# Kernel tuning notes

Measured on AMD Instinct MI355X. Metric: run time of the kernel, lower is better.

Reference implementation:

```python
import jax, jax.numpy as jnp
import numpy as np
from jax import lax

B, T, I, H = 64, 512, 512, 1024


def setup_inputs() -> dict:
    key = jax.random.key(0)
    k1, k2, k3, k4 = jax.random.split(key, 4)
    # Gates stacked in order: resetgate, updategate, hidden_update (matches forward()).
    inp = jax.random.normal(k1, (B, T, I), dtype=jnp.float32)
    W_in_stacked = jax.random.normal(k2, (I, 3 * H), dtype=jnp.float32) * 0.1
    W_hid_stacked = jax.random.normal(k3, (H, 3 * H), dtype=jnp.float32) * 0.1
    b_stacked = jax.random.normal(k4, (3 * H,), dtype=jnp.float32) * 0.1
    hid_init = jnp.zeros((1, H), dtype=jnp.float32)
    return {"inp": inp, "W_in_stacked": W_in_stacked,
            "W_hid_stacked": W_hid_stacked, "b_stacked": b_stacked,
            "hid_init": hid_init}


def reference(inp, W_in_stacked, W_hid_stacked, b_stacked, hid_init):
    n_units = hid_init.shape[1]
    n_batch = inp.shape[0]
    # Precompute the input contribution for all timesteps (as the original does
    # with one big mm before the loop): [B,T,3H] -> [T,B,3H] seq-first.
    x = jnp.einsum('bti,ig->btg', inp, W_in_stacked) + b_stacked
    x = jnp.swapaxes(x, 0, 1)
    h0 = jnp.broadcast_to(hid_init, (n_batch, n_units))

    def step(h_prev, x_t):
        hid_input = h_prev @ W_hid_stacked  # [B, 3H]
        r = jax.nn.sigmoid(x_t[:, :n_units] + hid_input[:, :n_units])
        u = jax.nn.sigmoid(x_t[:, n_units:2 * n_units]
                           + hid_input[:, n_units:2 * n_units])
        c = jnp.tanh(x_t[:, 2 * n_units:] + r * hid_input[:, 2 * n_units:])
        h_new = (1.0 - u) * h_prev + u * c
        return h_new, None

    h_final, _ = lax.scan(step, h0, x)
    return h_final  # [B, n_units]
```

## Files before the change

### kernel.cpp

```cpp
#include <hip/hip_runtime.h>
#include <hip/hip_fp16.h>

typedef _Float16 h16;
typedef __attribute__((ext_vector_type(4))) _Float16 h16x4;
typedef __attribute__((ext_vector_type(8))) _Float16 h16x8;
typedef __attribute__((ext_vector_type(4))) float f32x4;
typedef unsigned long long u64;

#define T_SEQ 512
#define NB    64
#define NI    512
#define NH    1024
#define N3H   3072

__device__ __forceinline__ u64 cload64(const u64* p) {
  return __hip_atomic_load(p, __ATOMIC_RELAXED, __HIP_MEMORY_SCOPE_AGENT);
}
__device__ __forceinline__ void cstore64(u64* p, u64 v) {
  __hip_atomic_store(p, v, __ATOMIC_RELAXED, __HIP_MEMORY_SCOPE_AGENT);
}

union H4 { u64 q; h16x4 v; };

__global__ void gru_init_h(const float* __restrict__ hid0,
                           h16* __restrict__ hfrag) {
  int t = blockIdx.x * blockDim.x + threadIdx.x;
  if (t >= 4 * 2048) return;
  int bg = t >> 11;
  int fl = t & 2047;
  int l  = fl & 63;
  int kbase = (fl >> 6) * 32 + (l >> 4) * 8;
  h16x8 v;
  #pragma unroll
  for (int j = 0; j < 8; ++j) v[j] = (h16)hid0[kbase + j];
  *(h16x8*)&hfrag[((size_t)bg * 2048 + fl) * 8] = v;
}

#define P1_BM 128
#define P1_BK 32

__device__ __forceinline__ int p1swz(int r, int k) {
  return r * P1_BK + ((((k >> 3) ^ (r & 3)) << 3) | (k & 7));
}

__global__ __launch_bounds__(256, 2) void gru_xgemm(
    const float* __restrict__ inp, const float* __restrict__ Win,
    const float* __restrict__ bstk, h16* __restrict__ x) {
  __shared__ h16 sAh[2][P1_BM * P1_BK];
  __shared__ h16 sAl[2][P1_BM * P1_BK];
  __shared__ h16 sBh[2][P1_BM * P1_BK];
  __shared__ h16 sBl[2][P1_BM * P1_BK];

  const int tid = threadIdx.x;
  const int l = tid & 63;
  const int w = tid >> 6;
  const int wm = (w >> 1) * 64, wn = (w & 1) * 64;
  const int mi = blockIdx.x, ni = blockIdx.y;

  const int sr  = tid >> 1;
  const int skh = (tid & 1) * 16;

  const float* aSrcBase = inp + (size_t)(sr & 63) * (T_SEQ * NI)
                              + (size_t)(mi * 2 + (sr >> 6)) * NI + skh;
  const float* bSrcBase = Win + (size_t)skh * N3H + ni * 128 + sr;

  f32x4 acc[4][4] = {};
  float aReg[16];
  float bReg[16];

  auto stage_load = [&](int ks) {
    const float* ap = aSrcBase + ks * P1_BK;
    #pragma unroll
    for (int jg = 0; jg < 4; ++jg) {
      f32x4 v = *(const f32x4*)(ap + jg * 4);
      aReg[jg*4+0] = v[0]; aReg[jg*4+1] = v[1];
      aReg[jg*4+2] = v[2]; aReg[jg*4+3] = v[3];
    }
    const float* bp = bSrcBase + (size_t)ks * P1_BK * N3H;
    #pragma unroll
    for (int j = 0; j < 16; ++j) bReg[j] = bp[(size_t)j * N3H];
  };

  auto stage_write = [&](int buf) {
    #pragma unroll
    for (int jg = 0; jg < 4; ++jg) {
      int idx = p1swz(sr, skh + jg * 4);
      h16x4 hi, lo;
      #pragma unroll
      for (int j = 0; j < 4; ++j) {
        float v = aReg[jg*4+j];
        h16 h = (h16)v; hi[j] = h; lo[j] = (h16)(v - (float)h);
      }
      *(h16x4*)&sAh[buf][idx] = hi;
      *(h16x4*)&sAl[buf][idx] = lo;
      #pragma unroll
      for (int j = 0; j < 4; ++j) {
        float v = bReg[jg*4+j];
        h16 h = (h16)v; hi[j] = h; lo[j] = (h16)(v - (float)h);
      }
      *(h16x4*)&sBh[buf][idx] = hi;
      *(h16x4*)&sBl[buf][idx] = lo;
    }
  };

  auto compute = [&](int buf) {
    const int k0 = (l >> 4) * 8;
    h16x8 bh[4], bl[4];
    #pragma unroll
    for (int nt = 0; nt < 4; ++nt) {
      int idx = p1swz(wn + nt * 16 + (l & 15), k0);
      bh[nt] = *(const h16x8*)&sBh[buf][idx];
      bl[nt] = *(const h16x8*)&sBl[buf][idx];
    }
    #pragma unroll
    for (int mt = 0; mt < 4; ++mt) {
      int idx = p1swz(wm + mt * 16 + (l & 15), k0);
      h16x8 ah = *(const h16x8*)&sAh[buf][idx];
      h16x8 al = *(const h16x8*)&sAl[buf][idx];
      #pragma unroll
      for (int nt = 0; nt < 4; ++nt) {
        acc[mt][nt] = __builtin_amdgcn_mfma_f32_16x16x32_f16(ah, bh[nt], acc[mt][nt], 0, 0, 0);
        acc[mt][nt] = __builtin_amdgcn_mfma_f32_16x16x32_f16(ah, bl[nt], acc[mt][nt], 0, 0, 0);
        acc[mt][nt] = __builtin_amdgcn_mfma_f32_16x16x32_f16(al, bh[nt], acc[mt][nt], 0, 0, 0);
      }
    }
  };

  stage_load(0);
  stage_write(0);
  __syncthreads();
  for (int ks = 0; ks < 16; ++ks) {
    int buf = ks & 1;
    if (ks < 15) stage_load(ks + 1);
    compute(buf);
    if (ks < 15) stage_write(buf ^ 1);
    __syncthreads();
  }

  const int t = mi * 2 + (wm >> 6);
  const int rrb = (l >> 4) * 4;
  #pragma unroll
  for (int nt = 0; nt < 4; ++nt) {
    int colhi = ni * 8 + (wn >> 4) + nt;
    int gg  = colhi >> 6;
    int cgx = colhi & 63;
    float bias = bstk[(colhi << 4) + (l & 15)];
    #pragma unroll
    for (int mt = 0; mt < 4; ++mt) {
      h16x4 v;
      #pragma unroll
      for (int i = 0; i < 4; ++i) v[i] = (h16)(acc[mt][nt][i] + bias);
      size_t idx = ((((size_t)t * 3 + gg) * 64 + cgx) * 4 + mt) * 256
                 + (size_t)(l & 15) * 16 + rrb;
      *(h16x4*)&x[idx] = v;
    }
  }
}

__global__ __launch_bounds__(192, 1) void gru_steps(
    const float* __restrict__ Whid,
    const h16* __restrict__ x,
    h16* __restrict__ hfrag,
    unsigned* __restrict__ cnt,
    const float* __restrict__ hid0,
    float* __restrict__ out) {
  __shared__ h16 U[3 * 32 * 64 * 8];
  __shared__ h16 hstage[16384];
  __shared__ float rbuf[2][16 * 17];
  __shared__ float ubuf[2][16 * 17];
  __shared__ h16 tbuf[16 * 20];

  const int tid = threadIdx.x;
  const int l = tid & 63;
  const int g = tid >> 6;
  const int cg = blockIdx.x & 63;
  const int bg = blockIdx.x >> 6;

  {
    const float* base = Whid + (size_t)g * NH + (size_t)cg * 16 + (l & 15);
    for (int kt = 0; kt < 32; ++kt) {
      const float* src = base + (size_t)(kt * 32 + (l >> 4) * 8) * N3H;
      h16x8 v;
      #pragma unroll
      for (int j = 0; j < 8; ++j) v[j] = (h16)src[(size_t)j * N3H];
      *(h16x8*)&U[(size_t)((g * 32 + kt) * 64 + l) * 8] = v;
    }
  }

  const int rr0 = (l >> 4) * 4, cc = l & 15;

  float hq[4];
  if (g == 2) {
    float h0 = hid0[cg * 16 + cc];
    #pragma unroll
    for (int i = 0; i < 4; ++i) hq[i] = h0;
  }
  __syncthreads();

  const char* xb = (const char*)(x
      + ((((size_t)g * 64 + cg) * 4 + bg) * 256)
      + (size_t)cc * 16 + rr0);
  u64 xq = *(const u64*)xb;

  const h16* Ug = &U[(size_t)g * 32 * 64 * 8];
  u64* hfU64 = (u64*)hfrag;
  unsigned* mycnt = cnt + bg * 32;

  for (int s = 1; s <= T_SEQ; ++s) {
    const unsigned need = 64u * (unsigned)(s - 1);
    int spincnt = 0;
    for (;;) {
      unsigned v = __hip_atomic_load(mycnt, __ATOMIC_RELAXED,
                                     __HIP_MEMORY_SCOPE_AGENT);
      if (__builtin_amdgcn_readfirstlane(v) >= need) break;
      __builtin_amdgcn_s_sleep(1);
      if (++spincnt > 200000) break;
    }
    __builtin_amdgcn_sched_barrier(0);

    u64 xq_next = xq;
    if (s < T_SEQ) xq_next = *(const u64*)(xb + (size_t)s * 393216);

    const u64* src = hfU64 + ((size_t)((s - 1) & 1) * 4 + bg) * 4096;
    u64 tmp[22];
    #pragma unroll
    for (int k = 0; k < 22; ++k) {
      int wd = tid + 192 * k;
      tmp[k] = (wd < 4096) ? cload64(src + wd) : 0;
    }
    #pragma unroll
    for (int k = 0; k < 22; ++k) {
      int wd = tid + 192 * k;
      if (wd < 4096) ((u64*)hstage)[wd] = tmp[k];
    }
    __syncthreads();

    f32x4 a0 = {}, a1 = {};
    #pragma unroll
    for (int kt = 0; kt < 32; ++kt) {
      h16x8 a = *(const h16x8*)&hstage[(kt * 64 + l) * 8];
      h16x8 b = *(const h16x8*)&Ug[(kt * 64 + l) * 8];
      if (kt & 1) a1 = __builtin_amdgcn_mfma_f32_16x16x32_f16(a, b, a1, 0, 0, 0);
      else        a0 = __builtin_amdgcn_mfma_f32_16x16x32_f16(a, b, a0, 0, 0, 0);
    }
    f32x4 hid;
    #pragma unroll
    for (int i = 0; i < 4; ++i) hid[i] = a0[i] + a1[i];

    H4 xc; xc.q = xq;
    const int p = s & 1;

    if (g == 0) {
      #pragma unroll
      for (int i = 0; i < 4; ++i) {
        float pr = (float)xc.v[i] + hid[i];
        rbuf[p][(rr0 + i) * 17 + cc] = 1.0f / (1.0f + __expf(-pr));
      }
    } else if (g == 1) {
      #pragma unroll
      for (int i = 0; i < 4; ++i) {
        float pu = (float)xc.v[i] + hid[i];
        ubuf[p][(rr0 + i) * 17 + cc] = 1.0f / (1.0f + __expf(-pu));
      }
    }
    __syncthreads();

    if (g == 2) {
      #pragma unroll
      for (int i = 0; i < 4; ++i) {
        int rr = rr0 + i;
        float r = rbuf[p][rr * 17 + cc];
        float u = ubuf[p][rr * 17 + cc];
        float c = tanhf((float)xc.v[i] + r * hid[i]);
        float hn = (1.0f - u) * hq[i] + u * c;
        hq[i] = hn;
        tbuf[rr * 20 + cc] = (h16)hn;
        if (s == T_SEQ) out[(size_t)(bg * 16 + rr) * NH + cg * 16 + cc] = hn;
      }
      u64 blk = *(const u64*)&tbuf[((l >> 1) & 15) * 20
                                   + (l >> 5) * 8 + (l & 1) * 4];
      u64* dst = hfU64 + (((size_t)(s & 1) * 4 + bg) * 4096) + cg * 64 + l;
      cstore64(dst, blk);
      asm volatile("s_waitcnt vmcnt(0)" ::: "memory");
      if (l == 0)
        (void)__hip_atomic_fetch_add(mycnt, 1u, __ATOMIC_RELAXED,
                                     __HIP_MEMORY_SCOPE_AGENT);
    }
    xq = xq_next;
  }
}

extern "C" void kernel_launch(void* const* d_in, const int* in_sizes, int n_in,
                              void* d_out, int out_size, void* d_ws, size_t ws_size,
                              hipStream_t stream) {
  const float* inp  = (const float*)d_in[0];
  const float* Win  = (const float*)d_in[1];
  const float* Whid = (const float*)d_in[2];
  const float* bstk = (const float*)d_in[3];
  const float* hid0 = (const float*)d_in[4];
  float* out = (float*)d_out;

  char* ws = (char*)d_ws;
  const size_t xBytes = (size_t)T_SEQ * NB * N3H * sizeof(h16);
  const size_t hBytes = (size_t)2 * 4 * 16384 * sizeof(h16);
  const size_t cBytes = 4 * 32 * sizeof(unsigned);
  if (ws_size < xBytes + hBytes + cBytes) return;

  h16* x = (h16*)ws;
  h16* hfrag = (h16*)(ws + xBytes);
  unsigned* cnt = (unsigned*)(ws + xBytes + hBytes);

  hipMemsetAsync(cnt, 0, cBytes, stream);

  gru_init_h<<<dim3(8192 / 256), dim3(256), 0, stream>>>(hid0, hfrag);

  dim3 g1(32768 / P1_BM, N3H / 128);
  gru_xgemm<<<g1, dim3(256), 0, stream>>>(inp, Win, bstk, x);

  gru_steps<<<dim3(256), dim3(192), 0, stream>>>(Whid, x, hfrag, cnt, hid0, out);
}
```

Before: 2.730 ms.

## Use single-wave per block, per-block step tags, and direct register h loads

The recurrent step kernel now retires two of its three waves after staging the weights, and one wave computes all three gate MFMAs per k-tile. That removes the LDS rbuf/ubuf exchange and both per-step __syncthreads. The shared atomic counter is replaced with per-producer tag words that each consumer lane polls, and the hidden state is read straight from global memory into registers instead of being staged through LDS. tanh becomes an exp-based formula. This shortens the per-step critical path of barriers and LDS round trips, at the cost of three times the MFMA work serialized in one wave, higher register pressure (64 u64 A values), and a less-parallel epilogue.

```diff
diff --git a/kernel.cpp b/kernel.cpp
--- a/kernel.cpp
+++ b/kernel.cpp
@@ -1,5 +1,6 @@
 #include <hip/hip_runtime.h>
 #include <hip/hip_fp16.h>
+#include <math.h>
 
 typedef _Float16 h16;
 typedef __attribute__((ext_vector_type(4))) _Float16 h16x4;
@@ -19,21 +20,31 @@
 __device__ __forceinline__ void cstore64(u64* p, u64 v) {
   __hip_atomic_store(p, v, __ATOMIC_RELAXED, __HIP_MEMORY_SCOPE_AGENT);
 }
+__device__ __forceinline__ unsigned cload32(const unsigned* p) {
+  return __hip_atomic_load(p, __ATOMIC_RELAXED, __HIP_MEMORY_SCOPE_AGENT);
+}
+__device__ __forceinline__ void cstore32(unsigned* p, unsigned v) {
+  __hip_atomic_store(p, v, __ATOMIC_RELAXED, __HIP_MEMORY_SCOPE_AGENT);
+}
 
 union H4 { u64 q; h16x4 v; };
+union F8 { u64 q[2]; h16x8 v; };
+
 
 __global__ void gru_init_h(const float* __restrict__ hid0,
-                           h16* __restrict__ hfrag) {
-  int t = blockIdx.x * blockDim.x + threadIdx.x;
-  if (t >= 4 * 2048) return;
-  int bg = t >> 11;
-  int fl = t & 2047;
-  int l  = fl & 63;
-  int kbase = (fl >> 6) * 32 + (l >> 4) * 8;
-  h16x8 v;
+                           u64* __restrict__ hfrag) {
+  int W = blockIdx.x * blockDim.x + threadIdx.x;
+  if (W >= 16384) return;
+  int bg = W >> 12;
+  int w  = W & 4095;
+  int kt = w >> 7;
+  int lp = (w >> 1) & 63;
+  int q  = w & 1;
+  int cb = kt * 32 + ((lp >> 4) & 3) * 8 + q * 4;
+  H4 o;
   #pragma unroll
-  for (int j = 0; j < 8; ++j) v[j] = (h16)hid0[kbase + j];
-  *(h16x8*)&hfrag[((size_t)bg * 2048 + fl) * 8] = v;
+  for (int j = 0; j < 4; ++j) o.v[j] = (h16)hid0[cb + j];
+  hfrag[(size_t)bg * 4096 + w] = o.q;
 }
 
 #define P1_BM 128
@@ -160,15 +171,12 @@
 __global__ __launch_bounds__(192, 1) void gru_steps(
     const float* __restrict__ Whid,
     const h16* __restrict__ x,
-    h16* __restrict__ hfrag,
-    unsigned* __restrict__ cnt,
+    u64* __restrict__ hfrag,
+    unsigned* __restrict__ tags,
     const float* __restrict__ hid0,
     float* __restrict__ out) {
   __shared__ h16 U[3 * 32 * 64 * 8];
-  __shared__ h16 hstage[16384];
-  __shared__ float rbuf[2][16 * 17];
-  __shared__ float ubuf[2][16 * 17];
-  __shared__ h16 tbuf[16 * 20];
+  __shared__ h16 tq[16 * 20];
 
   const int tid = threadIdx.x;
   const int l = tid & 63;
@@ -186,107 +194,94 @@
       *(h16x8*)&U[(size_t)((g * 32 + kt) * 64 + l) * 8] = v;
     }
   }
+  __syncthreads();
+  if (g != 0) return;
 
   const int rr0 = (l >> 4) * 4, cc = l & 15;
 
   float hq[4];
-  if (g == 2) {
+  {
     float h0 = hid0[cg * 16 + cc];
     #pragma unroll
     for (int i = 0; i < 4; ++i) hq[i] = h0;
   }
-  __syncthreads();
-
-  const char* xb = (const char*)(x
-      + ((((size_t)g * 64 + cg) * 4 + bg) * 256)
-      + (size_t)cc * 16 + rr0);
-  u64 xq = *(const u64*)xb;
-
-  const h16* Ug = &U[(size_t)g * 32 * 64 * 8];
-  u64* hfU64 = (u64*)hfrag;
-  unsigned* mycnt = cnt + bg * 32;
+
+  const char* xb0 = (const char*)(x + ((((size_t)0 * 64 + cg) * 4 + bg) * 256)
+                                    + (size_t)cc * 16 + rr0);
+  const char* xb1 = xb0 + 64 * 4 * 256 * 2;
+  const char* xb2 = xb1 + 64 * 4 * 256 * 2;
+  u64 xq0 = *(const u64*)xb0, xq1 = *(const u64*)xb1, xq2 = *(const u64*)xb2;
+
+  const int dstw = cg * 64 + ((l >> 4) >> 1) * 32 + (l & 15) * 2 + ((l >> 4) & 1);
 
   for (int s = 1; s <= T_SEQ; ++s) {
-    const unsigned need = 64u * (unsigned)(s - 1);
-    int spincnt = 0;
-    for (;;) {
-      unsigned v = __hip_atomic_load(mycnt, __ATOMIC_RELAXED,
-                                     __HIP_MEMORY_SCOPE_AGENT);
-      if (__builtin_amdgcn_readfirstlane(v) >= need) break;
-      __builtin_amdgcn_s_sleep(1);
-      if (++spincnt > 200000) break;
+    const int par = (s - 1) & 1;
+    const u64* plane = hfrag + ((size_t)par * 4 + bg) * 4096;
+    const unsigned* tgin = tags + (par * 4 + bg) * 64;
+
+    {
+      const unsigned need = (unsigned)(s - 1);
+      int spincnt = 0;
+      for (;;) {
+        unsigned tv = cload32(tgin + l);
+        if (__all((int)(tv >= need))) break;
+        __builtin_amdgcn_s_sleep(1);
+        if (++spincnt > 200000) break;
+      }
     }
     __builtin_amdgcn_sched_barrier(0);
 
-    u64 xq_next = xq;
-    if (s < T_SEQ) xq_next = *(const u64*)(xb + (size_t)s * 393216);
-
-    const u64* src = hfU64 + ((size_t)((s - 1) & 1) * 4 + bg) * 4096;
-    u64 tmp[22];
-    #pragma unroll
-    for (int k = 0; k < 22; ++k) {
-      int wd = tid + 192 * k;
-      tmp[k] = (wd < 4096) ? cload64(src + wd) : 0;
-    }
-    #pragma unroll
-    for (int k = 0; k < 22; ++k) {
-      int wd = tid + 192 * k;
-      if (wd < 4096) ((u64*)hstage)[wd] = tmp[k];
-    }
-    __syncthreads();
-
-    f32x4 a0 = {}, a1 = {};
+    u64 xn0 = xq0, xn1 = xq1, xn2 = xq2;
+    if (s < T_SEQ) {
+      xn0 = *(const u64*)(xb0 + (size_t)s * 393216);
+      xn1 = *(const u64*)(xb1 + (size_t)s * 393216);
+      xn2 = *(const u64*)(xb2 + (size_t)s * 393216);
+    }
+
+    u64 A[64];
     #pragma unroll
     for (int kt = 0; kt < 32; ++kt) {
-      h16x8 a = *(const h16x8*)&hstage[(kt * 64 + l) * 8];
-      h16x8 b = *(const h16x8*)&Ug[(kt * 64 + l) * 8];
-      if (kt & 1) a1 = __builtin_amdgcn_mfma_f32_16x16x32_f16(a, b, a1, 0, 0, 0);
-      else        a0 = __builtin_amdgcn_mfma_f32_16x16x32_f16(a, b, a0, 0, 0, 0);
-    }
-    f32x4 hid;
-    #pragma unroll
-    for (int i = 0; i < 4; ++i) hid[i] = a0[i] + a1[i];
-
-    H4 xc; xc.q = xq;
-    const int p = s & 1;
-
-    if (g == 0) {
-      #pragma unroll
-      for (int i = 0; i < 4; ++i) {
-        float pr = (float)xc.v[i] + hid[i];
-        rbuf[p][(rr0 + i) * 17 + cc] = 1.0f / (1.0f + __expf(-pr));
-      }
-    } else if (g == 1) {
-      #pragma unroll
-      for (int i = 0; i < 4; ++i) {
-        float pu = (float)xc.v[i] + hid[i];
-        ubuf[p][(rr0 + i) * 17 + cc] = 1.0f / (1.0f + __expf(-pu));
-      }
-    }
-    __syncthreads();
-
-    if (g == 2) {
-      #pragma unroll
-      for (int i = 0; i < 4; ++i) {
-        int rr = rr0 + i;
-        float r = rbuf[p][rr * 17 + cc];
-        float u = ubuf[p][rr * 17 + cc];
-        float c = tanhf((float)xc.v[i] + r * hid[i]);
-        float hn = (1.0f - u) * hq[i] + u * c;
-        hq[i] = hn;
-        tbuf[rr * 20 + cc] = (h16)hn;
-        if (s == T_SEQ) out[(size_t)(bg * 16 + rr) * NH + cg * 16 + cc] = hn;
-      }
-      u64 blk = *(const u64*)&tbuf[((l >> 1) & 15) * 20
-                                   + (l >> 5) * 8 + (l & 1) * 4];
-      u64* dst = hfU64 + (((size_t)(s & 1) * 4 + bg) * 4096) + cg * 64 + l;
-      cstore64(dst, blk);
-      asm volatile("s_waitcnt vmcnt(0)" ::: "memory");
-      if (l == 0)
-        (void)__hip_atomic_fetch_add(mycnt, 1u, __ATOMIC_RELAXED,
-                                     __HIP_MEMORY_SCOPE_AGENT);
-    }
-    xq = xq_next;
+      A[2 * kt]     = cload64(plane + ((size_t)kt * 64 + l) * 2);
+      A[2 * kt + 1] = cload64(plane + ((size_t)kt * 64 + l) * 2 + 1);
+    }
+
+    f32x4 ac0 = {}, ac1 = {}, ac2 = {};
+    #pragma unroll
+    for (int kt = 0; kt < 32; ++kt) {
+      F8 f; f.q[0] = A[2 * kt]; f.q[1] = A[2 * kt + 1];
+      h16x8 b0 = *(const h16x8*)&U[(size_t)((0 * 32 + kt) * 64 + l) * 8];
+      h16x8 b1 = *(const h16x8*)&U[(size_t)((1 * 32 + kt) * 64 + l) * 8];
+      h16x8 b2 = *(const h16x8*)&U[(size_t)((2 * 32 + kt) * 64 + l) * 8];
+      ac0 = __builtin_amdgcn_mfma_f32_16x16x32_f16(f.v, b0, ac0, 0, 0, 0);
+      ac1 = __builtin_amdgcn_mfma_f32_16x16x32_f16(f.v, b1, ac1, 0, 0, 0);
+      ac2 = __builtin_amdgcn_mfma_f32_16x16x32_f16(f.v, b2, ac2, 0, 0, 0);
+    }
+
+    H4 xr; xr.q = xq0;
+    H4 xu; xu.q = xq1;
+    H4 xc; xc.q = xq2;
+    #pragma unroll
+    for (int i = 0; i < 4; ++i) {
+      float r = 1.0f / (1.0f + __expf(-((float)xr.v[i] + ac0[i])));
+      float u = 1.0f / (1.0f + __expf(-((float)xu.v[i] + ac1[i])));
+      float z = (float)xc.v[i] + r * ac2[i];
+      float e = __expf(2.0f * z);
+      float c = 1.0f - 2.0f / (e + 1.0f);
+      float hn = (1.0f - u) * hq[i] + u * c;
+      hq[i] = hn;
+      tq[(rr0 + i) * 20 + cc] = (h16)hn;
+      if (s == T_SEQ) out[(size_t)(bg * 16 + rr0 + i) * NH + cg * 16 + cc] = hn;
+    }
+
+    H4 pv; pv.v = *(const h16x4*)&tq[(l & 15) * 20 + (l >> 4) * 4];
+    u64* outp = hfrag + ((size_t)(s & 1) * 4 + bg) * 4096;
+    cstore64(outp + dstw, pv.q);
+    asm volatile("s_waitcnt vmcnt(0)" ::: "memory");
+    __builtin_amdgcn_sched_barrier(0);
+    if (l == 0)
+      cstore32(tags + ((s & 1) * 4 + bg) * 64 + cg, (unsigned)s);
+
+    xq0 = xn0; xq1 = xn1; xq2 = xn2;
   }
 }
 
@@ -302,20 +297,20 @@
 
   char* ws = (char*)d_ws;
   const size_t xBytes = (size_t)T_SEQ * NB * N3H * sizeof(h16);
-  const size_t hBytes = (size_t)2 * 4 * 16384 * sizeof(h16);
-  const size_t cBytes = 4 * 32 * sizeof(unsigned);
-  if (ws_size < xBytes + hBytes + cBytes) return;
+  const size_t hBytes = (size_t)2 * 4 * 4096 * sizeof(u64);
+  const size_t tBytes = 2 * 4 * 64 * sizeof(unsigned);
+  if (ws_size < xBytes + hBytes + tBytes) return;
 
   h16* x = (h16*)ws;
-  h16* hfrag = (h16*)(ws + xBytes);
-  unsigned* cnt = (unsigned*)(ws + xBytes + hBytes);
-
-  hipMemsetAsync(cnt, 0, cBytes, stream);
-
-  gru_init_h<<<dim3(8192 / 256), dim3(256), 0, stream>>>(hid0, hfrag);
+  u64* hfrag = (u64*)(ws + xBytes);
+  unsigned* tags = (unsigned*)(ws + xBytes + hBytes);
+
+  hipMemsetAsync(tags, 0, tBytes, stream);
+
+  gru_init_h<<<dim3(16384 / 256), dim3(256), 0, stream>>>(hid0, hfrag);
 
   dim3 g1(32768 / P1_BM, N3H / 128);
   gru_xgemm<<<g1, dim3(256), 0, stream>>>(inp, Win, bstk, x);
 
-  gru_steps<<<dim3(256), dim3(192), 0, stream>>>(Whid, x, hfrag, cnt, hid0, out);
-}
+  gru_steps<<<dim3(256), dim3(192), 0, stream>>>(Whid, x, hfrag, tags, hid0, out);
+}
```

Measured after the change: 2.548 ms. -6.7%, faster.
